# Kernel optimization log

Hardware: AMD Instinct MI355X
Metric: run time of the kernel (lower is better)

Reference implementation:

```python
import jax, jax.numpy as jnp
import numpy as np

N, F, B = 4096, 2048, 2048


def setup_inputs() -> dict:
    key = jax.random.key(0)
    ks = jax.random.split(key, 11)
    s_h = 1.0 / np.sqrt(F).astype(np.float32)
    s_x = 1.0 / np.sqrt(B).astype(np.float32)
    inp = {
        "behavior": jax.random.normal(ks[0], (N, B), jnp.float32),
        "h0": jax.random.normal(ks[1], (N, F), jnp.float32),
        "c0": jax.random.normal(ks[2], (N, F), jnp.float32),
        "Wi_h": jax.random.normal(ks[3], (F, F), jnp.float32) * s_h,
        "Wi_x": jax.random.normal(ks[4], (B, F), jnp.float32) * s_x,
        "bi": jnp.zeros((F,), jnp.float32),
        "Wf_h": jax.random.normal(ks[5], (F, F), jnp.float32) * s_h,
        "Wf_x": jax.random.normal(ks[6], (B, F), jnp.float32) * s_x,
        "bf": jnp.zeros((F,), jnp.float32),
        "Wg_h": jax.random.normal(ks[7], (F, F), jnp.float32) * s_h,
        "Wg_x": jax.random.normal(ks[8], (B, F), jnp.float32) * s_x,
        "bg": jnp.zeros((F,), jnp.float32),
        "Wo_h": jax.random.normal(ks[9], (F, F), jnp.float32) * s_h,
        "Wo_x": jax.random.normal(ks[10], (B, F), jnp.float32) * s_x,
        "bo": jnp.zeros((F,), jnp.float32),
    }
    return inp


def reference(behavior, h0, c0, Wi_h, Wi_x, bi, Wf_h, Wf_x, bf,
              Wg_h, Wg_x, bg, Wo_h, Wo_x, bo):
    # Single-step LSTM cell: each gate is a two-input linear proj (h, behavior)
    def proj(Wh, Wx, b):
        return h0 @ Wh + behavior @ Wx + b  # [N, F]

    i = jax.nn.sigmoid(proj(Wi_h, Wi_x, bi))
    f = jax.nn.sigmoid(proj(Wf_h, Wf_x, bf))
    g = jnp.tanh(proj(Wg_h, Wg_x, bg))
    o = jax.nn.sigmoid(proj(Wo_h, Wo_x, bo))
    c = f * c0 + i * g
    h = o * jnp.tanh(c)
    return h
```

## Files before the change

### kernel.cpp

```cpp
#include <hip/hip_runtime.h>
#include <stdint.h>

#define N_ROWS 4096
#define F_DIM  2048
#define B_DIM  2048
#define K_DIM  4096

typedef __attribute__((ext_vector_type(8)))  __bf16 bf16x8;
typedef __attribute__((ext_vector_type(16))) float  f32x16;
typedef unsigned short u16;

__device__ __forceinline__ u16 f2bf(float x) {
  unsigned int u = __float_as_uint(x);
  u += 0x7fffu + ((u >> 16) & 1u);
  return (u16)(u >> 16);
}

__device__ __forceinline__ void async_copy16(const void* g, void* l) {
  __builtin_amdgcn_global_load_lds(
      (const __attribute__((address_space(1))) void*)g,
      (__attribute__((address_space(3))) void*)l, 16, 0, 0);
}

__device__ __forceinline__ float sigmoid_f(float x) {
  return 1.0f / (1.0f + __expf(-x));
}
__device__ __forceinline__ float tanh_f(float x) {
  float e2 = __expf(2.0f * x);
  return 1.0f - 2.0f / (e2 + 1.0f);
}

__global__ __launch_bounds__(256) void pack_x_kernel(
    const float* __restrict__ h0, const float* __restrict__ behavior,
    u16* __restrict__ Xc)
{
  int tid = blockIdx.x * 256 + threadIdx.x;
  int row = tid >> 9;
  int k0  = (tid & 511) * 8;
  const float* src = (k0 < F_DIM) ? (h0 + (size_t)row * F_DIM + k0)
                                  : (behavior + (size_t)row * B_DIM + (k0 - F_DIM));
  const float4* s4 = (const float4*)src;
  float4 a = s4[0], b = s4[1];
  uint4 o;
  o.x = (unsigned)f2bf(a.x) | ((unsigned)f2bf(a.y) << 16);
  o.y = (unsigned)f2bf(a.z) | ((unsigned)f2bf(a.w) << 16);
  o.z = (unsigned)f2bf(b.x) | ((unsigned)f2bf(b.y) << 16);
  o.w = (unsigned)f2bf(b.z) | ((unsigned)f2bf(b.w) << 16);
  *(uint4*)(Xc + (size_t)tid * 8) = o;
}

__global__ __launch_bounds__(256) void pack_w_kernel(
    const float* __restrict__ wi_h, const float* __restrict__ wi_x,
    const float* __restrict__ wf_h, const float* __restrict__ wf_x,
    const float* __restrict__ wg_h, const float* __restrict__ wg_x,
    const float* __restrict__ wo_h, const float* __restrict__ wo_x,
    u16* __restrict__ WT)
{
  __shared__ float tileT[32 * 65];
  int g = blockIdx.z;
  const float* Wh = (g == 0) ? wi_h : (g == 1) ? wf_h : (g == 2) ? wg_h : wo_h;
  const float* Wx = (g == 0) ? wi_x : (g == 1) ? wf_x : (g == 2) ? wg_x : wo_x;
  int fb = blockIdx.x * 32;
  int kb = blockIdx.y * 64;
  const float* W = (kb < F_DIM) ? Wh : Wx;
  int kofs = (kb < F_DIM) ? kb : (kb - F_DIM);

  int t  = threadIdx.x;
  int c4 = t & 7;
  int kr = t >> 3;
#pragma unroll
  for (int p = 0; p < 2; ++p) {
    int k_l = kr + p * 32;
    float4 v = *(const float4*)(W + (size_t)(kofs + k_l) * F_DIM + fb + c4 * 4);
    tileT[(c4 * 4 + 0) * 65 + k_l] = v.x;
    tileT[(c4 * 4 + 1) * 65 + k_l] = v.y;
    tileT[(c4 * 4 + 2) * 65 + k_l] = v.z;
    tileT[(c4 * 4 + 3) * 65 + k_l] = v.w;
  }
  __syncthreads();
  {
    int f_l = t >> 3;
    int k8  = (t & 7) * 8;
    const float* s = tileT + f_l * 65 + k8;
    uint4 o;
    o.x = (unsigned)f2bf(s[0]) | ((unsigned)f2bf(s[1]) << 16);
    o.y = (unsigned)f2bf(s[2]) | ((unsigned)f2bf(s[3]) << 16);
    o.z = (unsigned)f2bf(s[4]) | ((unsigned)f2bf(s[5]) << 16);
    o.w = (unsigned)f2bf(s[6]) | ((unsigned)f2bf(s[7]) << 16);
    *(uint4*)(WT + ((size_t)g * F_DIM + fb + f_l) * K_DIM + kb + k8) = o;
  }
}

__global__ __launch_bounds__(256, 2) void lstm_gemm_kernel(
    const u16* __restrict__ Xc, const u16* __restrict__ WT,
    const float* __restrict__ c0,
    const float* __restrict__ bi, const float* __restrict__ bff,
    const float* __restrict__ bg, const float* __restrict__ bo,
    float* __restrict__ out)
{
  __shared__ u16 As[128 * 64];
  __shared__ u16 Bs[4 * 64 * 64];

  const int tid  = threadIdx.x;
  const int lane = tid & 63;
  const int wv   = tid >> 6;
  const int bm   = blockIdx.x;
  const int bn   = blockIdx.y;

  const int rw = wv & 1;
  const int fh = wv >> 1;
  const int l31  = lane & 31;
  const int half = lane >> 5;

  const u16* agp[4];
  const u16* bgp[8];
#pragma unroll
  for (int j = 0; j < 4; ++j) {
    int c = j * 256 + tid;
    int r = c >> 3, o = (c & 7) ^ (r & 7);
    agp[j] = Xc + (size_t)(bm * 128 + r) * K_DIM + o * 8;
  }
#pragma unroll
  for (int g = 0; g < 4; ++g)
#pragma unroll
    for (int jj = 0; jj < 2; ++jj) {
      int c = jj * 256 + tid;
      int r = c >> 3, o = (c & 7) ^ (r & 7);
      bgp[g * 2 + jj] = WT + ((size_t)g * F_DIM + bn * 64 + r) * K_DIM + o * 8;
    }
  const unsigned ubase = (unsigned)(tid & ~63) * 16u;

  f32x16 acc[4][2];
#pragma unroll
  for (int g = 0; g < 4; ++g)
#pragma unroll
    for (int rh = 0; rh < 2; ++rh)
#pragma unroll
      for (int r = 0; r < 16; ++r) acc[g][rh][r] = 0.f;

  for (int kt = 0; kt < 64; ++kt) {
#pragma unroll
    for (int j = 0; j < 4; ++j)
      async_copy16(agp[j], (char*)As + j * 4096 + ubase);
#pragma unroll
    for (int j = 0; j < 8; ++j)
      async_copy16(bgp[j], (char*)Bs + (j >> 1) * 8192 + (j & 1) * 4096 + ubase);
#pragma unroll
    for (int j = 0; j < 4; ++j) agp[j] += 64;
#pragma unroll
    for (int j = 0; j < 8; ++j) bgp[j] += 64;
    __syncthreads();

#pragma unroll
    for (int c = 0; c < 4; ++c) {
      const int oct = c * 2 + half;
      const int sw  = oct ^ (l31 & 7);
      bf16x8 af[2];
#pragma unroll
      for (int rh = 0; rh < 2; ++rh) {
        int m = rw * 64 + rh * 32 + l31;
        af[rh] = *(const bf16x8*)(As + m * 64 + sw * 8);
      }
      bf16x8 bfr[4];
#pragma unroll
      for (int g = 0; g < 4; ++g) {
        int fl = fh * 32 + l31;
        bfr[g] = *(const bf16x8*)(Bs + g * 4096 + fl * 64 + sw * 8);
      }
#pragma unroll
      for (int g = 0; g < 4; ++g)
#pragma unroll
        for (int rh = 0; rh < 2; ++rh)
          acc[g][rh] = __builtin_amdgcn_mfma_f32_32x32x16_bf16(
              af[rh], bfr[g], acc[g][rh], 0, 0, 0);
    }
    __syncthreads();
  }

  {
    int f = bn * 64 + fh * 32 + l31;
    float b0 = bi[f], b1 = bff[f], b2 = bg[f], b3 = bo[f];
#pragma unroll
    for (int rh = 0; rh < 2; ++rh) {
      int row_base = bm * 128 + rw * 64 + rh * 32 + 4 * half;
#pragma unroll
      for (int r = 0; r < 16; ++r) {
        int row = row_base + (r & 3) + 8 * (r >> 2);
        size_t idx = (size_t)row * F_DIM + f;
        float pi = acc[0][rh][r] + b0;
        float pf = acc[1][rh][r] + b1;
        float pg = acc[2][rh][r] + b2;
        float po = acc[3][rh][r] + b3;
        float iv = sigmoid_f(pi);
        float fv = sigmoid_f(pf);
        float gv = tanh_f(pg);
        float ov = sigmoid_f(po);
        float cv = fv * c0[idx] + iv * gv;
        out[idx] = ov * tanh_f(cv);
      }
    }
  }
}

extern "C" void kernel_launch(void* const* d_in, const int* in_sizes, int n_in,
                              void* d_out, int out_size, void* d_ws, size_t ws_size,
                              hipStream_t stream) {
  const float* behavior = (const float*)d_in[0];
  const float* h0       = (const float*)d_in[1];
  const float* c0       = (const float*)d_in[2];
  const float* Wi_h     = (const float*)d_in[3];
  const float* Wi_x     = (const float*)d_in[4];
  const float* bi       = (const float*)d_in[5];
  const float* Wf_h     = (const float*)d_in[6];
  const float* Wf_x     = (const float*)d_in[7];
  const float* bf       = (const float*)d_in[8];
  const float* Wg_h     = (const float*)d_in[9];
  const float* Wg_x     = (const float*)d_in[10];
  const float* bg       = (const float*)d_in[11];
  const float* Wo_h     = (const float*)d_in[12];
  const float* Wo_x     = (const float*)d_in[13];
  const float* bo       = (const float*)d_in[14];
  float* out = (float*)d_out;

  u16* Xc = (u16*)d_ws;
  u16* WT = Xc + (size_t)N_ROWS * K_DIM;

  pack_x_kernel<<<dim3(N_ROWS * (K_DIM / 8) / 256), 256, 0, stream>>>(h0, behavior, Xc);
  pack_w_kernel<<<dim3(F_DIM / 32, K_DIM / 64, 4), 256, 0, stream>>>(
      Wi_h, Wi_x, Wf_h, Wf_x, Wg_h, Wg_x, Wo_h, Wo_x, WT);
  lstm_gemm_kernel<<<dim3(N_ROWS / 128, F_DIM / 64), 256, 0, stream>>>(
      Xc, WT, c0, bi, bf, bg, bo, out);
}
```

Baseline: 508.8 us.

## Double-buffer LDS tiles with BK=32 to overlap global loads with MFMA

Splits the K tile from 64 to 32 and allocates two LDS buffers for the A and B tiles. The next tile's async global-to-LDS copies are issued before computing on the current one, with the swizzle reworked for 32-wide rows. The aim is to hide global load latency that the single-buffered loop exposed at every iteration. This doubles the number of iterations and barriers, and a new LDS swizzle pattern may add bank conflicts.

```diff
diff --git a/kernel.cpp b/kernel.cpp
--- a/kernel.cpp
+++ b/kernel.cpp
@@ -5,6 +5,7 @@
 #define F_DIM  2048
 #define B_DIM  2048
 #define K_DIM  4096
+#define BK     32
 
 typedef __attribute__((ext_vector_type(8)))  __bf16 bf16x8;
 typedef __attribute__((ext_vector_type(16))) float  f32x16;
@@ -98,8 +99,8 @@
     const float* __restrict__ bg, const float* __restrict__ bo,
     float* __restrict__ out)
 {
-  __shared__ u16 As[128 * 64];
-  __shared__ u16 Bs[4 * 64 * 64];
+  __shared__ u16 As[2][128 * BK];
+  __shared__ u16 Bs[2][4 * 64 * BK];
 
   const int tid  = threadIdx.x;
   const int lane = tid & 63;
@@ -112,61 +113,74 @@
   const int l31  = lane & 31;
   const int half = lane >> 5;
 
-  const u16* agp[4];
-  const u16* bgp[8];
+  const u16* agp[2];
+  const u16* bgp[4];
+#pragma unroll
+  for (int j = 0; j < 2; ++j) {
+    int c = j * 256 + tid;
+    int r = c >> 2, o = (c & 3) ^ ((r >> 1) & 3);
+    agp[j] = Xc + (size_t)(bm * 128 + r) * K_DIM + o * 8;
+  }
 #pragma unroll
   for (int j = 0; j < 4; ++j) {
     int c = j * 256 + tid;
-    int r = c >> 3, o = (c & 7) ^ (r & 7);
-    agp[j] = Xc + (size_t)(bm * 128 + r) * K_DIM + o * 8;
-  }
+    int r = c >> 2, o = (c & 3) ^ ((r >> 1) & 3);
+    int g = r >> 6, fl = r & 63;
+    bgp[j] = WT + ((size_t)g * F_DIM + bn * 64 + fl) * K_DIM + o * 8;
+  }
+  const unsigned ubase = (unsigned)(tid & ~63) * 16u;
+
+  f32x16 acc[4][2];
 #pragma unroll
   for (int g = 0; g < 4; ++g)
 #pragma unroll
-    for (int jj = 0; jj < 2; ++jj) {
-      int c = jj * 256 + tid;
-      int r = c >> 3, o = (c & 7) ^ (r & 7);
-      bgp[g * 2 + jj] = WT + ((size_t)g * F_DIM + bn * 64 + r) * K_DIM + o * 8;
+    for (int rh = 0; rh < 2; ++rh)
+#pragma unroll
+      for (int r = 0; r < 16; ++r) acc[g][rh][r] = 0.f;
+
+#pragma unroll
+  for (int j = 0; j < 2; ++j)
+    async_copy16(agp[j], (char*)As[0] + j * 4096 + ubase);
+#pragma unroll
+  for (int j = 0; j < 4; ++j)
+    async_copy16(bgp[j], (char*)Bs[0] + j * 4096 + ubase);
+#pragma unroll
+  for (int j = 0; j < 2; ++j) agp[j] += BK;
+#pragma unroll
+  for (int j = 0; j < 4; ++j) bgp[j] += BK;
+  __syncthreads();
+
+  const int swq = (l31 >> 1) & 3;
+  const int mrow = rw * 64 + l31;
+  const int frow = fh * 32 + l31;
+
+  for (int kt = 0; kt < 128; ++kt) {
+    const int p = kt & 1;
+    if (kt + 1 < 128) {
+#pragma unroll
+      for (int j = 0; j < 2; ++j)
+        async_copy16(agp[j], (char*)As[p ^ 1] + j * 4096 + ubase);
+#pragma unroll
+      for (int j = 0; j < 4; ++j)
+        async_copy16(bgp[j], (char*)Bs[p ^ 1] + j * 4096 + ubase);
+#pragma unroll
+      for (int j = 0; j < 2; ++j) agp[j] += BK;
+#pragma unroll
+      for (int j = 0; j < 4; ++j) bgp[j] += BK;
     }
-  const unsigned ubase = (unsigned)(tid & ~63) * 16u;
-
-  f32x16 acc[4][2];
-#pragma unroll
-  for (int g = 0; g < 4; ++g)
-#pragma unroll
-    for (int rh = 0; rh < 2; ++rh)
-#pragma unroll
-      for (int r = 0; r < 16; ++r) acc[g][rh][r] = 0.f;
-
-  for (int kt = 0; kt < 64; ++kt) {
-#pragma unroll
-    for (int j = 0; j < 4; ++j)
-      async_copy16(agp[j], (char*)As + j * 4096 + ubase);
-#pragma unroll
-    for (int j = 0; j < 8; ++j)
-      async_copy16(bgp[j], (char*)Bs + (j >> 1) * 8192 + (j & 1) * 4096 + ubase);
-#pragma unroll
-    for (int j = 0; j < 4; ++j) agp[j] += 64;
-#pragma unroll
-    for (int j = 0; j < 8; ++j) bgp[j] += 64;
-    __syncthreads();
-
-#pragma unroll
-    for (int c = 0; c < 4; ++c) {
-      const int oct = c * 2 + half;
-      const int sw  = oct ^ (l31 & 7);
+
+#pragma unroll
+    for (int c16 = 0; c16 < 2; ++c16) {
+      const int oct = c16 * 2 + half;
+      const int sw  = oct ^ swq;
       bf16x8 af[2];
 #pragma unroll
-      for (int rh = 0; rh < 2; ++rh) {
-        int m = rw * 64 + rh * 32 + l31;
-        af[rh] = *(const bf16x8*)(As + m * 64 + sw * 8);
-      }
+      for (int rh = 0; rh < 2; ++rh)
+        af[rh] = *(const bf16x8*)(&As[p][(mrow + rh * 32) * BK + sw * 8]);
       bf16x8 bfr[4];
 #pragma unroll
-      for (int g = 0; g < 4; ++g) {
-        int fl = fh * 32 + l31;
-        bfr[g] = *(const bf16x8*)(Bs + g * 4096 + fl * 64 + sw * 8);
-      }
+      for (int g = 0; g < 4; ++g)
+        bfr[g] = *(const bf16x8*)(&Bs[p][(g * 64 + frow) * BK + sw * 8]);
 #pragma unroll
       for (int g = 0; g < 4; ++g)
 #pragma unroll
```

Measured after the change: 576.8 us. 13.3% more time.
